# Kernel optimization log

Hardware: AMD Instinct MI355X
Metric: run time of the kernel (lower is better)

Reference implementation:

```python
import jax, jax.numpy as jnp
import numpy as np

GAMMA = 0.99
EPS = 1e-07


def setup_inputs() -> dict:
    key = jax.random.key(0)
    k1, k2, k3 = jax.random.split(key, 3)
    V, D = 8192, 256
    b, s = 8, 16
    x = jax.random.normal(k1, (b, D, s, s, s), dtype=jnp.float32)
    weight = jax.random.normal(k2, (V, D), dtype=jnp.float32)
    N = jnp.zeros((V,), dtype=jnp.float32)
    z_avg = jax.random.normal(k3, (V, D), dtype=jnp.float32)
    return {"x": x, "weight": weight, "N": N, "z_avg": z_avg}


def reference(x, weight, N, z_avg):
    V, D = weight.shape
    b, c, x1, x2, x3 = x.shape
    # (b, c, x1, x2, x3) -> (b*x1*x2*x3, D), channels last
    flat = jnp.transpose(x, (0, 2, 3, 4, 1)).reshape(-1, D)
    # pairwise squared L2 distances: ||z||^2 - 2 z.W^T + ||W||^2
    dists = (
        jnp.sum(flat * flat, axis=1, keepdims=True)
        - 2.0 * (flat @ weight.T)
        + jnp.sum(weight * weight, axis=1)[None, :]
    )
    idx = jnp.argmin(dists, axis=1)  # same tie-break (first) as torch.max(-d)
    quant = weight[idx].reshape(b, x1, x2, x3, D)
    quant = jnp.transpose(quant, (0, 4, 1, 2, 3))  # back to (b, c, x1, x2, x3)

    # EMA cluster statistics (training-mode update) via scatter-reduce,
    # equivalent to the torch one-hot matmuls encode_onehot.sum(0) and
    # flat_inputs.T @ encode_onehot.
    counts = jax.ops.segment_sum(jnp.ones(flat.shape[0], dtype=flat.dtype), idx, num_segments=V)
    enc_sum = jax.ops.segment_sum(flat, idx, num_segments=V)  # (V, D)
    new_N = GAMMA * N + (1.0 - GAMMA) * counts
    new_z_avg = GAMMA * z_avg + (1.0 - GAMMA) * enc_sum
    n = jnp.sum(new_N)
    w = (new_N + EPS) / (n + V * EPS) * n
    new_weight = new_z_avg / w[:, None]

    quant_st = jax.lax.stop_gradient(quant - x) + x  # straight-through
    quant_diff = jnp.mean(jnp.square(x - jax.lax.stop_gradient(quant)))
    enc_idx = idx.reshape(b, x1, x2, x3)
    return quant_st, enc_idx, quant_diff, new_N, new_z_avg, new_weight
```

## Files before the change

kernel.cpp:

```cpp
#include <hip/hip_runtime.h>

#define V_CODES 8192
#define D_DIM   256
#define SPATIAL 4096
#define M_ROWS  32768
#define NELEM   8388608

static constexpr float GAMMA_F = 0.99f;
static constexpr float OMG_F   = (float)(1.0 - 0.99);
static constexpr float EPS_F   = 1e-7f;
static constexpr float VEPS_F  = (float)(8192 * 1e-7);

static constexpr size_t OFF_QUANT = 0;
static constexpr size_t OFF_IDX   = 8388608;
static constexpr size_t OFF_QDIFF = 8421376;
static constexpr size_t OFF_NN    = 8421377;
static constexpr size_t OFF_ZAVG  = 8429569;
static constexpr size_t OFF_W     = 10526721;

typedef _Float16 f16x8  __attribute__((ext_vector_type(8)));
typedef _Float16 f16x4  __attribute__((ext_vector_type(4)));
typedef float    f32x4  __attribute__((ext_vector_type(4)));

#define GLL(gp, lp) __builtin_amdgcn_global_load_lds( \
    (const __attribute__((address_space(1))) unsigned int*)(gp), \
    (__attribute__((address_space(3))) unsigned int*)(lp), 16, 0, 0)

__global__ void k_split_w(const float* __restrict__ W, _Float16* __restrict__ Wh,
                          _Float16* __restrict__ Wl, float* __restrict__ wnorm) {
    int t = threadIdx.x;
    size_t i8 = ((size_t)blockIdx.x * 256 + t) * 8;
    float4 a = *(const float4*)(W + i8);
    float4 b = *(const float4*)(W + i8 + 4);
    float v[8] = {a.x, a.y, a.z, a.w, b.x, b.y, b.z, b.w};
    f16x8 hi, lo;
    float ns = 0.0f;
    #pragma unroll
    for (int j = 0; j < 8; j++) {
        _Float16 h = (_Float16)v[j];
        hi[j] = h;
        lo[j] = (_Float16)(v[j] - (float)h);
        ns = fmaf(v[j], v[j], ns);
    }
    *(f16x8*)(Wh + i8) = hi;
    *(f16x8*)(Wl + i8) = lo;
    #pragma unroll
    for (int m = 16; m > 0; m >>= 1) ns += __shfl_xor(ns, m, 64);
    if ((t & 31) == 0) wnorm[blockIdx.x * 8 + (t >> 5)] = ns;
}

__global__ void k_split_x(const float* __restrict__ X, _Float16* __restrict__ Xh,
                          _Float16* __restrict__ Xl) {
    int bid  = blockIdx.x;
    int lane = threadIdx.x & 63;
    int kg   = (bid & 1) * 4 + (threadIdx.x >> 6);
    int m    = (bid >> 1) * 64 + lane;
    int b  = m >> 12;
    int sp = m & 4095;
    const float* src = X + (size_t)b * (D_DIM * SPATIAL) + (size_t)(kg * 32) * SPATIAL + sp;
    float v[32];
    #pragma unroll
    for (int j = 0; j < 32; j++) v[j] = src[(size_t)j * SPATIAL];
    _Float16* dh = Xh + (size_t)m * D_DIM + kg * 32;
    _Float16* dl = Xl + (size_t)m * D_DIM + kg * 32;
    #pragma unroll
    for (int c = 0; c < 4; c++) {
        f16x8 hi, lo;
        #pragma unroll
        for (int j = 0; j < 8; j++) {
            float x = v[c * 8 + j];
            _Float16 h = (_Float16)x;
            hi[j] = h;
            lo[j] = (_Float16)(x - (float)h);
        }
        *(f16x8*)(dh + c * 8) = hi;
        *(f16x8*)(dl + c * 8) = lo;
    }
}

__device__ inline unsigned long long packkey(float s, int v) {
    unsigned u = __float_as_uint(s);
    u = (u & 0x80000000u) ? ~u : (u | 0x80000000u);
    return ((unsigned long long)u << 32) | (unsigned)v;
}

__global__ __launch_bounds__(256, 2) void k_mfma_argmin(
        const _Float16* __restrict__ Xh, const _Float16* __restrict__ Xl,
        const _Float16* __restrict__ Wh, const _Float16* __restrict__ Wl,
        const float* __restrict__ wnorm, unsigned long long* __restrict__ best) {
    __shared__ __align__(16) _Float16 lds[24576];
    const int tid  = threadIdx.x;
    const int wid  = tid >> 6;
    const int lane = tid & 63;
    const int lrow = lane & 15, lq = lane >> 4;
    const int wy = wid >> 1, wx = wid & 1;
    const int m0 = blockIdx.y * 128;
    const int v0 = blockIdx.x * 256;

    const _Float16* const planes[4] = {Xh, Xl, Wh, Wl};

    const _Float16* gp[12];
    #pragma unroll
    for (int j = 0; j < 12; ++j) {
        int ss = wid * 12 + j;
        int pl = (ss >= 8) + (ss >= 16) + (ss >= 32);
        int ro = ss - (pl == 1 ? 8 : pl == 2 ? 16 : pl == 3 ? 32 : 0);
        gp[j] = planes[pl] + (size_t)((pl < 2 ? m0 : v0) + ro * 16 + lrow) * D_DIM + lq * 8;
    }

    f32x4 acc[4][8] = {};

    for (int k0 = 0; k0 < D_DIM; k0 += 32) {
        __syncthreads();
        #pragma unroll
        for (int j = 0; j < 12; ++j)
            GLL(gp[j] + k0, &lds[(wid * 12 + j) * 512]);
        __syncthreads();
        f16x8 ah[4], al[4];
        #pragma unroll
        for (int i = 0; i < 4; ++i) {
            ah[i] = *(const f16x8*)&lds[(     wy * 4 + i) * 512 + lane * 8];
            al[i] = *(const f16x8*)&lds[(8 +  wy * 4 + i) * 512 + lane * 8];
        }
        #pragma unroll
        for (int h = 0; h < 4; ++h) {
            f16x8 bh[2], bl[2];
            #pragma unroll
            for (int i = 0; i < 2; ++i) {
                bh[i] = *(const f16x8*)&lds[(16 + wx * 8 + h * 2 + i) * 512 + lane * 8];
                bl[i] = *(const f16x8*)&lds[(32 + wx * 8 + h * 2 + i) * 512 + lane * 8];
            }
            __builtin_amdgcn_s_setprio(1);
            #pragma unroll
            for (int mi = 0; mi < 4; ++mi)
                #pragma unroll
                for (int vj = 0; vj < 2; ++vj) {
                    acc[mi][h*2+vj] = __builtin_amdgcn_mfma_f32_16x16x32_f16(ah[mi], bh[vj], acc[mi][h*2+vj], 0, 0, 0);
                    acc[mi][h*2+vj] = __builtin_amdgcn_mfma_f32_16x16x32_f16(al[mi], bh[vj], acc[mi][h*2+vj], 0, 0, 0);
                    acc[mi][h*2+vj] = __builtin_amdgcn_mfma_f32_16x16x32_f16(ah[mi], bl[vj], acc[mi][h*2+vj], 0, 0, 0);
                }
            __builtin_amdgcn_s_setprio(0);
        }
    }

    float wnv[8];
    #pragma unroll
    for (int vi = 0; vi < 8; ++vi) wnv[vi] = wnorm[v0 + (wx * 8 + vi) * 16 + lrow];

    #pragma unroll
    for (int mi = 0; mi < 4; ++mi) {
        #pragma unroll
        for (int r = 0; r < 4; ++r) {
            unsigned long long k = ~0ull;
            #pragma unroll
            for (int vi = 0; vi < 8; ++vi) {
                int v = v0 + (wx * 8 + vi) * 16 + lrow;
                float s = wnv[vi] - 2.0f * acc[mi][vi][r];
                unsigned long long key = packkey(s, v);
                k = key < k ? key : k;
            }
            #pragma unroll
            for (int msk = 1; msk < 16; msk <<= 1) {
                unsigned long long o = __shfl_xor(k, msk, 64);
                k = o < k ? o : k;
            }
            if (lrow == 0) {
                int m = m0 + (wy * 4 + mi) * 16 + lq * 4 + r;
                atomicMin(&best[m], k);
            }
        }
    }
}

__global__ void k_count(const unsigned long long* __restrict__ best,
                        int* __restrict__ counts, float* __restrict__ out) {
    int m = blockIdx.x * 256 + threadIdx.x;
    int v = (int)(unsigned)(best[m] & 0xFFFFFFFFull);
    atomicAdd(&counts[v], 1);
    out[OFF_IDX + m] = (float)v;
}

__global__ void k_prefix(const int* __restrict__ counts, int* __restrict__ offsets,
                         int* __restrict__ cursor) {
    __shared__ int tsum[256];
    int t = threadIdx.x;
    int local[32];
    int s = 0;
    #pragma unroll
    for (int i = 0; i < 32; i++) { local[i] = s; s += counts[t * 32 + i]; }
    tsum[t] = s;
    __syncthreads();
    if (t == 0) {
        int run = 0;
        for (int i = 0; i < 256; i++) { int c = tsum[i]; tsum[i] = run; run += c; }
    }
    __syncthreads();
    int base = tsum[t];
    #pragma unroll
    for (int i = 0; i < 32; i++) {
        int o = base + local[i];
        offsets[t * 32 + i] = o;
        cursor[t * 32 + i]  = o;
    }
}

__global__ void k_fill(const unsigned long long* __restrict__ best,
                       int* __restrict__ cursor, int* __restrict__ bin) {
    int m = blockIdx.x * 256 + threadIdx.x;
    int v = (int)(unsigned)(best[m] & 0xFFFFFFFFull);
    int pos = atomicAdd(&cursor[v], 1);
    bin[pos] = m;
}

__global__ void k_codes(const _Float16* __restrict__ Xh, const _Float16* __restrict__ Xl,
                        const float* __restrict__ N, const float* __restrict__ zavg,
                        const int* __restrict__ counts, const int* __restrict__ offsets,
                        const int* __restrict__ bin, float* __restrict__ out,
                        float* __restrict__ ws_scal) {
    int v = blockIdx.x;
    int t = threadIdx.x;
    int r4 = t >> 6;
    int dg = t & 63;
    int cnt = counts[v];
    int off = offsets[v];
    float s0 = 0.f, s1 = 0.f, s2 = 0.f, s3 = 0.f;
    for (int r = r4; r < cnt; r += 4) {
        int m = bin[off + r];
        f16x4 h = *(const f16x4*)(Xh + (size_t)m * D_DIM + dg * 4);
        f16x4 l = *(const f16x4*)(Xl + (size_t)m * D_DIM + dg * 4);
        s0 += (float)h[0] + (float)l[0];
        s1 += (float)h[1] + (float)l[1];
        s2 += (float)h[2] + (float)l[2];
        s3 += (float)h[3] + (float)l[3];
    }
    __shared__ float red[4][256];
    *(float4*)&red[r4][dg * 4] = make_float4(s0, s1, s2, s3);
    __syncthreads();
    float tot = red[0][t] + red[1][t] + red[2][t] + red[3][t];
    out[OFF_ZAVG + (size_t)v * D_DIM + t] = GAMMA_F * zavg[(size_t)v * D_DIM + t] + OMG_F * tot;
    if (t == 0) {
        float nn = GAMMA_F * N[v] + OMG_F * (float)cnt;
        out[OFF_NN + v] = nn;
        atomicAdd(&ws_scal[1], nn);
    }
}

__global__ void k_quant(const float* __restrict__ X, const float* __restrict__ W,
                        const unsigned long long* __restrict__ best, float* __restrict__ out,
                        float* __restrict__ ws_scal) {
    int e4 = blockIdx.x * 256 + threadIdx.x;
    int e  = e4 * 4;
    int sp = e & 4095;
    int bd = e >> 12;
    int d  = bd & 255;
    int b  = bd >> 8;
    int mb = b * SPATIAL + sp;
    float4 x4 = *(const float4*)(X + e);
    float q[4];
    float p = 0.0f;
    #pragma unroll
    for (int j = 0; j < 4; j++) {
        int v = (int)(unsigned)(best[mb + j] & 0xFFFFFFFFull);
        float wv = W[(size_t)v * D_DIM + d];
        float xv = (j == 0) ? x4.x : (j == 1) ? x4.y : (j == 2) ? x4.z : x4.w;
        q[j] = (wv - xv) + xv;
        float df = xv - wv;
        p = fmaf(df, df, p);
    }
    *(float4*)(out + OFF_QUANT + e) = make_float4(q[0], q[1], q[2], q[3]);
    #pragma unroll
    for (int msk = 32; msk > 0; msk >>= 1) p += __shfl_xor(p, msk, 64);
    __shared__ float red[4];
    int lane = threadIdx.x & 63, w = threadIdx.x >> 6;
    if (lane == 0) red[w] = p;
    __syncthreads();
    if (threadIdx.x == 0)
        atomicAdd(ws_scal, red[0] + red[1] + red[2] + red[3]);
}

__global__ void k_weight(const float* __restrict__ zavg_out, const float* __restrict__ nn_out,
                         const float* __restrict__ ws_scal, float* __restrict__ out_w,
                         float* __restrict__ out_qdiff) {
    int i = blockIdx.x * 256 + threadIdx.x;
    if (i == 0) out_qdiff[0] = ws_scal[0] * (1.0f / 8388608.0f);
    int v = i >> 8;
    float n = ws_scal[1];
    float w = (nn_out[v] + EPS_F) / (n + VEPS_F) * n;
    out_w[i] = zavg_out[i] / w;
}

extern "C" void kernel_launch(void* const* d_in, const int* in_sizes, int n_in,
                              void* d_out, int out_size, void* d_ws, size_t ws_size,
                              hipStream_t stream) {
    const float* x    = (const float*)d_in[0];
    const float* w    = (const float*)d_in[1];
    const float* N    = (const float*)d_in[2];
    const float* zavg = (const float*)d_in[3];
    float* out = (float*)d_out;
    char*  wsb = (char*)d_ws;

    float* ws_scal   = (float*)wsb;
    int*   ws_counts = (int*)(wsb + 64);
    float* ws_wnorm  = (float*)(wsb + 32832);
    int*   ws_off    = (int*)(wsb + 65600);
    int*   ws_cur    = (int*)(wsb + 98368);
    int*   ws_bin    = (int*)(wsb + 131136);
    unsigned long long* ws_best = (unsigned long long*)(wsb + 262208);
    _Float16* Xh = (_Float16*)(wsb + 524352);
    _Float16* Xl = (_Float16*)(wsb + 524352 + 16777216);
    _Float16* Wh = (_Float16*)(wsb + 524352 + 2 * 16777216);
    _Float16* Wl = (_Float16*)(wsb + 524352 + 2 * 16777216 + 4194304);

    hipMemsetAsync(wsb, 0, 32832, stream);
    hipMemsetAsync(ws_best, 0xFF, (size_t)M_ROWS * 8, stream);

    k_split_w<<<(V_CODES * D_DIM) / (256 * 8), 256, 0, stream>>>(w, Wh, Wl, ws_wnorm);
    k_split_x<<<1024, 256, 0, stream>>>(x, Xh, Xl);

    dim3 grid(V_CODES / 256, M_ROWS / 128);
    k_mfma_argmin<<<grid, 256, 0, stream>>>(Xh, Xl, Wh, Wl, ws_wnorm, ws_best);

    k_count  <<<M_ROWS / 256, 256, 0, stream>>>(ws_best, ws_counts, out);
    k_prefix <<<1, 256, 0, stream>>>(ws_counts, ws_off, ws_cur);
    k_fill   <<<M_ROWS / 256, 256, 0, stream>>>(ws_best, ws_cur, ws_bin);
    k_codes  <<<V_CODES, 256, 0, stream>>>(Xh, Xl, N, zavg, ws_counts, ws_off, ws_bin, out, ws_scal);
    k_quant  <<<NELEM / (256 * 4), 256, 0, stream>>>(x, w, ws_best, out, ws_scal);

    k_weight <<<(V_CODES * D_DIM) / 256, 256, 0, stream>>>(out + OFF_ZAVG, out + OFF_NN, ws_scal,
                                                           out + OFF_W, out + OFF_QDIFF);
}
```

Before: 879.1 us.

## Enlarge argmin GEMM tile to 256x256 with 8 waves per block

The distance GEMM block tile grows from 128x256 to 256x256 rows by codes, using 512 threads arranged as 2x4 waves. Each wave now holds 8x4 accumulator tiles, and the loop is reordered so the B fragments are loaded once per k-step and A fragments are streamed. The intent is to halve W-plane global and LDS traffic per output and raise arithmetic intensity. In exchange, LDS grows to 64KB per block and 512 threads at 2 blocks per CU push register pressure, which may reduce occupancy or cause spills.

Result: slower. 1.060 ms (+20.5%).

```diff
diff --git a/kernel.cpp b/kernel.cpp
--- a/kernel.cpp
+++ b/kernel.cpp
@@ -84,77 +84,71 @@
     return ((unsigned long long)u << 32) | (unsigned)v;
 }
 
-__global__ __launch_bounds__(256, 2) void k_mfma_argmin(
+__global__ __launch_bounds__(512, 2) void k_mfma_argmin(
         const _Float16* __restrict__ Xh, const _Float16* __restrict__ Xl,
         const _Float16* __restrict__ Wh, const _Float16* __restrict__ Wl,
         const float* __restrict__ wnorm, unsigned long long* __restrict__ best) {
-    __shared__ __align__(16) _Float16 lds[24576];
+    __shared__ __align__(16) _Float16 lds[32768];
     const int tid  = threadIdx.x;
     const int wid  = tid >> 6;
     const int lane = tid & 63;
     const int lrow = lane & 15, lq = lane >> 4;
-    const int wy = wid >> 1, wx = wid & 1;
-    const int m0 = blockIdx.y * 128;
+    const int wy = wid >> 2, wx = wid & 3;
+    const int m0 = blockIdx.y * 256;
     const int v0 = blockIdx.x * 256;
 
     const _Float16* const planes[4] = {Xh, Xl, Wh, Wl};
 
-    const _Float16* gp[12];
-    #pragma unroll
-    for (int j = 0; j < 12; ++j) {
-        int ss = wid * 12 + j;
-        int pl = (ss >= 8) + (ss >= 16) + (ss >= 32);
-        int ro = ss - (pl == 1 ? 8 : pl == 2 ? 16 : pl == 3 ? 32 : 0);
+    const _Float16* gp[8];
+    #pragma unroll
+    for (int j = 0; j < 8; ++j) {
+        int ss = wid * 8 + j;
+        int pl = ss >> 4;
+        int ro = ss & 15;
         gp[j] = planes[pl] + (size_t)((pl < 2 ? m0 : v0) + ro * 16 + lrow) * D_DIM + lq * 8;
     }
 
-    f32x4 acc[4][8] = {};
+    f32x4 acc[8][4] = {};
 
     for (int k0 = 0; k0 < D_DIM; k0 += 32) {
         __syncthreads();
         #pragma unroll
-        for (int j = 0; j < 12; ++j)
-            GLL(gp[j] + k0, &lds[(wid * 12 + j) * 512]);
+        for (int j = 0; j < 8; ++j)
+            GLL(gp[j] + k0, &lds[(wid * 8 + j) * 512]);
         __syncthreads();
-        f16x8 ah[4], al[4];
+        f16x8 bh[4], bl[4];
         #pragma unroll
         for (int i = 0; i < 4; ++i) {
-            ah[i] = *(const f16x8*)&lds[(     wy * 4 + i) * 512 + lane * 8];
-            al[i] = *(const f16x8*)&lds[(8 +  wy * 4 + i) * 512 + lane * 8];
+            bh[i] = *(const f16x8*)&lds[(32 + wx * 4 + i) * 512 + lane * 8];
+            bl[i] = *(const f16x8*)&lds[(48 + wx * 4 + i) * 512 + lane * 8];
         }
         #pragma unroll
-        for (int h = 0; h < 4; ++h) {
-            f16x8 bh[2], bl[2];
-            #pragma unroll
-            for (int i = 0; i < 2; ++i) {
-                bh[i] = *(const f16x8*)&lds[(16 + wx * 8 + h * 2 + i) * 512 + lane * 8];
-                bl[i] = *(const f16x8*)&lds[(32 + wx * 8 + h * 2 + i) * 512 + lane * 8];
-            }
+        for (int mi = 0; mi < 8; ++mi) {
+            f16x8 ah = *(const f16x8*)&lds[(     wy * 8 + mi) * 512 + lane * 8];
+            f16x8 al = *(const f16x8*)&lds[(16 + wy * 8 + mi) * 512 + lane * 8];
             __builtin_amdgcn_s_setprio(1);
             #pragma unroll
-            for (int mi = 0; mi < 4; ++mi)
-                #pragma unroll
-                for (int vj = 0; vj < 2; ++vj) {
-                    acc[mi][h*2+vj] = __builtin_amdgcn_mfma_f32_16x16x32_f16(ah[mi], bh[vj], acc[mi][h*2+vj], 0, 0, 0);
-                    acc[mi][h*2+vj] = __builtin_amdgcn_mfma_f32_16x16x32_f16(al[mi], bh[vj], acc[mi][h*2+vj], 0, 0, 0);
-                    acc[mi][h*2+vj] = __builtin_amdgcn_mfma_f32_16x16x32_f16(ah[mi], bl[vj], acc[mi][h*2+vj], 0, 0, 0);
-                }
+            for (int vi = 0; vi < 4; ++vi) {
+                acc[mi][vi] = __builtin_amdgcn_mfma_f32_16x16x32_f16(ah, bh[vi], acc[mi][vi], 0, 0, 0);
+                acc[mi][vi] = __builtin_amdgcn_mfma_f32_16x16x32_f16(al, bh[vi], acc[mi][vi], 0, 0, 0);
+                acc[mi][vi] = __builtin_amdgcn_mfma_f32_16x16x32_f16(ah, bl[vi], acc[mi][vi], 0, 0, 0);
+            }
             __builtin_amdgcn_s_setprio(0);
         }
     }
 
-    float wnv[8];
-    #pragma unroll
-    for (int vi = 0; vi < 8; ++vi) wnv[vi] = wnorm[v0 + (wx * 8 + vi) * 16 + lrow];
-
-    #pragma unroll
-    for (int mi = 0; mi < 4; ++mi) {
+    float wnv[4];
+    #pragma unroll
+    for (int vi = 0; vi < 4; ++vi) wnv[vi] = wnorm[v0 + (wx * 4 + vi) * 16 + lrow];
+
+    #pragma unroll
+    for (int mi = 0; mi < 8; ++mi) {
         #pragma unroll
         for (int r = 0; r < 4; ++r) {
             unsigned long long k = ~0ull;
             #pragma unroll
-            for (int vi = 0; vi < 8; ++vi) {
-                int v = v0 + (wx * 8 + vi) * 16 + lrow;
+            for (int vi = 0; vi < 4; ++vi) {
+                int v = v0 + (wx * 4 + vi) * 16 + lrow;
                 float s = wnv[vi] - 2.0f * acc[mi][vi][r];
                 unsigned long long key = packkey(s, v);
                 k = key < k ? key : k;
@@ -165,7 +159,7 @@
                 k = o < k ? o : k;
             }
             if (lrow == 0) {
-                int m = m0 + (wy * 4 + mi) * 16 + lq * 4 + r;
+                int m = m0 + wy * 128 + mi * 16 + lq * 4 + r;
                 atomicMin(&best[m], k);
             }
         }
@@ -317,8 +311,8 @@
     k_split_w<<<(V_CODES * D_DIM) / (256 * 8), 256, 0, stream>>>(w, Wh, Wl, ws_wnorm);
     k_split_x<<<1024, 256, 0, stream>>>(x, Xh, Xl);
 
-    dim3 grid(V_CODES / 256, M_ROWS / 128);
-    k_mfma_argmin<<<grid, 256, 0, stream>>>(Xh, Xl, Wh, Wl, ws_wnorm, ws_best);
+    dim3 grid(V_CODES / 256, M_ROWS / 256);
+    k_mfma_argmin<<<grid, 512, 0, stream>>>(Xh, Xl, Wh, Wl, ws_wnorm, ws_best);
 
     k_count  <<<M_ROWS / 256, 256, 0, stream>>>(ws_best, ws_counts, out);
     k_prefix <<<1, 256, 0, stream>>>(ws_counts, ws_off, ws_cur);
```
